# Kernel optimization log

Hardware: AMD Instinct MI355X
Metric: run time of the kernel (lower is better)

## Reference

```python
import jax, jax.numpy as jnp
import numpy as np

B, N, HID = 8, 512, 512
HEADS, HD = 16, 32
FFN, DEMB = 2048, 64
EPS = 1e-5


def layer_norm(x, g, b):
    mu = jnp.mean(x, axis=-1, keepdims=True)
    var = jnp.var(x, axis=-1, keepdims=True)
    return (x - mu) * jax.lax.rsqrt(var + EPS) * g + b


def setup_inputs() -> dict:
    key = jax.random.key(0)
    ks = jax.random.split(key, 16)
    s = lambda fan_in: 1.0 / np.sqrt(fan_in)
    return {
        "x": jax.random.normal(ks[0], (B, N, HID), jnp.float32),
        "distance_features": jax.random.normal(ks[1], (B, N, N, DEMB), jnp.float32),
        "edge_mask": jax.random.randint(ks[2], (B, N, N), 0, 2) > 0,
        "qkv_w": jax.random.uniform(ks[3], (HID, 3 * HID), jnp.float32, -s(HID), s(HID)),
        "qkv_b": jnp.zeros((3 * HID,), jnp.float32),
        "out_w": jax.random.uniform(ks[4], (HID, HID), jnp.float32, -s(HID), s(HID)),
        "out_b": jnp.zeros((HID,), jnp.float32),
        "dist_w": jax.random.uniform(ks[5], (DEMB, HEADS), jnp.float32, -s(DEMB), s(DEMB)),
        "dist_b": jnp.zeros((HEADS,), jnp.float32),
        "ln1_g": jnp.ones((HID,), jnp.float32),
        "ln1_b": jnp.zeros((HID,), jnp.float32),
        "ln2_g": jnp.ones((HID,), jnp.float32),
        "ln2_b": jnp.zeros((HID,), jnp.float32),
        "ff1_w": jax.random.uniform(ks[6], (HID, FFN), jnp.float32, -s(HID), s(HID)),
        "ff1_b": jnp.zeros((FFN,), jnp.float32),
        "ff2_w": jax.random.uniform(ks[7], (FFN, HID), jnp.float32, -s(FFN), s(FFN)),
        "ff2_b": jnp.zeros((HID,), jnp.float32),
    }


def reference(x, distance_features, edge_mask, qkv_w, qkv_b, out_w, out_b,
              dist_w, dist_b, ln1_g, ln1_b, ln2_g, ln2_b,
              ff1_w, ff1_b, ff2_w, ff2_b):
    residual = x
    h = layer_norm(x, ln1_g, ln1_b)
    qkv = h @ qkv_w + qkv_b  # [B,N,3*HID]
    q, k, v = jnp.split(qkv, 3, axis=-1)
    q = q.reshape(B, N, HEADS, HD)
    k = k.reshape(B, N, HEADS, HD)
    v = v.reshape(B, N, HEADS, HD)
    scale = jnp.sqrt(jnp.float32(HD))
    scores = jnp.einsum('bihd,bjhd->bhij', q, k) / scale  # [B,H,N,N]
    bias = distance_features @ dist_w + dist_b  # [B,N,N,H]
    scores = scores + jnp.transpose(bias, (0, 3, 1, 2))
    neg = jnp.finfo(scores.dtype).min
    scores = jnp.where(edge_mask[:, None, :, :], scores, neg)
    attn = jax.nn.softmax(scores, axis=-1)
    ctx = jnp.einsum('bhij,bjhd->bihd', attn, v).reshape(B, N, HID)
    x = residual + ctx @ out_w + out_b
    y = layer_norm(x, ln2_g, ln2_b)
    ff = jax.nn.gelu(y @ ff1_w + ff1_b, approximate=False) @ ff2_w + ff2_b
    return x + ff
```

## Files before the change

kernel.cpp:

```cpp
#include <hip/hip_runtime.h>
#include <cstddef>
#include <cstdint>

#define B_     8
#define N_     512
#define HID_   512
#define HEADS_ 16
#define HD_    32
#define FFN_   2048
#define DEMB_  64
#define ROWS   (B_*N_)

typedef unsigned short u16;
typedef short bf16x8 __attribute__((ext_vector_type(8)));
typedef float f32x4  __attribute__((ext_vector_type(4)));
typedef short short8v __attribute__((ext_vector_type(8)));
typedef short short4v __attribute__((ext_vector_type(4)));

__device__ __forceinline__ u16 f2bf(float f) {
  unsigned u = __float_as_uint(f);
  u += 0x7fffu + ((u >> 16) & 1u);
  return (u16)(u >> 16);
}
__device__ __forceinline__ float bf2f(u16 b) {
  return __uint_as_float(((unsigned)b) << 16);
}

__device__ __forceinline__ void gload16(const void* g, void* l) {
  __builtin_amdgcn_global_load_lds(
      (const __attribute__((address_space(1))) unsigned int*)g,
      (__attribute__((address_space(3))) unsigned int*)l, 16, 0, 0);
}

__device__ __forceinline__ void wt_tile(const float* __restrict__ W,
                                        u16* __restrict__ Wt,
                                        int K, int N, int tt, int tid) {
  __shared__ float tile[32][33];
  const int nt = N / 32;
  const int n0 = (tt % nt) * 32, k0 = (tt / nt) * 32;
  const int tx = tid & 31, ty = tid >> 5;
  #pragma unroll
  for (int i = 0; i < 4; ++i)
    tile[ty + 8 * i][tx] = W[(size_t)(k0 + ty + 8 * i) * N + n0 + tx];
  __syncthreads();
  #pragma unroll
  for (int i = 0; i < 4; ++i) {
    const int n = ty + 8 * i;
    Wt[(size_t)(n0 + n) * K + k0 + tx] = f2bf(tile[tx][n]);
  }
}

__global__ __launch_bounds__(256) void prep_kernel(
    const float* __restrict__ qkv_w, const float* __restrict__ out_w,
    const float* __restrict__ ff1_w, const float* __restrict__ ff2_w,
    u16* __restrict__ qkv_wt, u16* __restrict__ out_wt,
    u16* __restrict__ ff1_wt, u16* __restrict__ ff2_wt,
    const unsigned char* __restrict__ mask, int* __restrict__ flag) {
  const int bid = blockIdx.x, t = threadIdx.x;
  if (bid < 768) {
    wt_tile(qkv_w, qkv_wt, HID_, 3 * HID_, bid, t);
  } else if (bid < 1024) {
    wt_tile(out_w, out_wt, HID_, HID_, bid - 768, t);
  } else if (bid < 2048) {
    wt_tile(ff1_w, ff1_wt, HID_, FFN_, bid - 1024, t);
  } else if (bid < 3072) {
    wt_tile(ff2_w, ff2_wt, FFN_, HID_, bid - 2048, t);
  } else {
    const int idx = (bid - 3072) * 256 + t;
    if ((idx & 3) != 0 && mask[idx] != 0) atomicOr(flag, 1);
  }
}

__global__ __launch_bounds__(256) void ln_kernel(const float* __restrict__ x,
                                                 const float* __restrict__ g,
                                                 const float* __restrict__ bt,
                                                 u16* __restrict__ y) {
  const int lane = threadIdx.x & 63;
  const int row  = blockIdx.x * 4 + (threadIdx.x >> 6);
  const float* xr = x + (size_t)row * HID_;
  float4 v0 = *(const float4*)(xr + lane * 8);
  float4 v1 = *(const float4*)(xr + lane * 8 + 4);
  float s = v0.x + v0.y + v0.z + v0.w + v1.x + v1.y + v1.z + v1.w;
  float q = v0.x*v0.x + v0.y*v0.y + v0.z*v0.z + v0.w*v0.w
          + v1.x*v1.x + v1.y*v1.y + v1.z*v1.z + v1.w*v1.w;
  #pragma unroll
  for (int off = 32; off > 0; off >>= 1) {
    s += __shfl_xor(s, off, 64);
    q += __shfl_xor(q, off, 64);
  }
  const float mean = s * (1.0f / HID_);
  const float var  = q * (1.0f / HID_) - mean * mean;
  const float rs   = rsqrtf(var + 1e-5f);
  const float4 g0 = *(const float4*)(g + lane * 8);
  const float4 g1 = *(const float4*)(g + lane * 8 + 4);
  const float4 b0 = *(const float4*)(bt + lane * 8);
  const float4 b1 = *(const float4*)(bt + lane * 8 + 4);
  short8v o;
  o[0] = (short)f2bf((v0.x - mean) * rs * g0.x + b0.x);
  o[1] = (short)f2bf((v0.y - mean) * rs * g0.y + b0.y);
  o[2] = (short)f2bf((v0.z - mean) * rs * g0.z + b0.z);
  o[3] = (short)f2bf((v0.w - mean) * rs * g0.w + b0.w);
  o[4] = (short)f2bf((v1.x - mean) * rs * g1.x + b1.x);
  o[5] = (short)f2bf((v1.y - mean) * rs * g1.y + b1.y);
  o[6] = (short)f2bf((v1.z - mean) * rs * g1.z + b1.z);
  o[7] = (short)f2bf((v1.w - mean) * rs * g1.w + b1.w);
  *(short8v*)(y + (size_t)row * HID_ + lane * 8) = o;
}

template <int ACT, bool HAS_RES, bool OUT_BF16>
__global__ __launch_bounds__(256) void mfma_gemm(
    const u16* __restrict__ A, const u16* __restrict__ Wt,
    const float* __restrict__ bias, const float* __restrict__ res,
    void* __restrict__ Cout, int N, int K) {
  __shared__ __align__(16) u16 As[128 * 64];
  __shared__ __align__(16) u16 Bs[128 * 64];
  const int t    = threadIdx.x;
  const int wid  = t >> 6, lane = t & 63;
  const int wr   = wid >> 1, wc = wid & 1;
  const int m0   = blockIdx.y * 128, n0 = blockIdx.x * 128;
  const int srow8 = lane >> 3;
  const int sslot = (lane & 7) ^ srow8;

  f32x4 zero = {0.f, 0.f, 0.f, 0.f};
  f32x4 acc[4][4];
  #pragma unroll
  for (int m = 0; m < 4; ++m)
    #pragma unroll
    for (int n = 0; n < 4; ++n) acc[m][n] = zero;

  for (int kt = 0; kt < K; kt += 64) {
    __syncthreads();
    #pragma unroll
    for (int i = 0; i < 4; ++i) {
      const int rbase = wid * 32 + i * 8;
      const int r = rbase + srow8;
      gload16(A  + (size_t)(m0 + r) * K + kt + sslot * 8, &As[rbase * 64]);
      gload16(Wt + (size_t)(n0 + r) * K + kt + sslot * 8, &Bs[rbase * 64]);
    }
    __syncthreads();
    #pragma unroll
    for (int kk = 0; kk < 2; ++kk) {
      bf16x8 a[4], b[4];
      #pragma unroll
      for (int m = 0; m < 4; ++m) {
        const int row = wr * 64 + m * 16 + (lane & 15);
        const int s   = (kk * 4 + (lane >> 4)) ^ (row & 7);
        a[m] = *(const bf16x8*)&As[row * 64 + s * 8];
      }
      #pragma unroll
      for (int n = 0; n < 4; ++n) {
        const int row = wc * 64 + n * 16 + (lane & 15);
        const int s   = (kk * 4 + (lane >> 4)) ^ (row & 7);
        b[n] = *(const bf16x8*)&Bs[row * 64 + s * 8];
      }
      #pragma unroll
      for (int m = 0; m < 4; ++m)
        #pragma unroll
        for (int n = 0; n < 4; ++n)
          acc[m][n] = __builtin_amdgcn_mfma_f32_16x16x32_bf16(
              a[m], b[n], acc[m][n], 0, 0, 0);
    }
  }
  #pragma unroll
  for (int n = 0; n < 4; ++n) {
    const int col = n0 + wc * 64 + n * 16 + (lane & 15);
    const float bb = bias[col];
    #pragma unroll
    for (int m = 0; m < 4; ++m) {
      #pragma unroll
      for (int j = 0; j < 4; ++j) {
        const int row = m0 + wr * 64 + m * 16 + (lane >> 4) * 4 + j;
        float v = acc[m][n][j] + bb;
        if (ACT == 1) v = 0.5f * v * (1.0f + erff(v * 0.70710678118654752f));
        const size_t off = (size_t)row * N + col;
        if (HAS_RES) v += res[off];
        if (OUT_BF16) ((u16*)Cout)[off] = f2bf(v);
        else          ((float*)Cout)[off] = v;
      }
    }
  }
}

__global__ __launch_bounds__(256) void bias_kernel(
    const float* __restrict__ df, const unsigned char* __restrict__ mask8,
    const float* __restrict__ dw, const float* __restrict__ db,
    const int* __restrict__ flag, u16* __restrict__ biasb) {
  __shared__ __align__(16) float dfs[128 * 64];
  __shared__ float wls[64 * 16];
  __shared__ float dbs[16];
  __shared__ unsigned char mbuf[128];
  __shared__ u16 obuf[16][132];

  const int t    = threadIdx.x;
  const int wid  = t >> 6, lane = t & 63;
  const int tile = blockIdx.x & 3;
  const int i    = (blockIdx.x >> 2) & 511;
  const int b    = blockIdx.x >> 11;
  const int j0   = tile * 128;

  const size_t dfbase = (((size_t)b * N_ + i) * N_ + j0) * DEMB_;
  #pragma unroll
  for (int s = 0; s < 8; ++s) {
    const int r0 = wid * 32 + s * 4;
    const int r  = r0 + (lane >> 4);
    const int g  = (lane & 15) ^ (r & 15);
    gload16(df + dfbase + (size_t)r * DEMB_ + g * 4, &dfs[r0 * 64]);
  }
  *(float4*)&wls[t * 4] = ((const float4*)dw)[t];
  if (t < 16) dbs[t] = db[t];
  const int fb = *flag;
  if (t < 128) {
    const size_t midx = ((size_t)b * N_ + i) * N_ + j0 + t;
    mbuf[t] = fb ? (mask8[midx] != 0) : (((const int*)mask8)[midx] != 0);
  }
  __syncthreads();

  bf16x8 bw[2];
  #pragma unroll
  for (int kk = 0; kk < 2; ++kk)
    #pragma unroll
    for (int e = 0; e < 8; ++e) {
      const int k = kk * 32 + (lane >> 4) * 8 + e;
      bw[kk][e] = (short)f2bf(wls[k * 16 + (lane & 15)]);
    }

  f32x4 acc[2] = {{0.f,0.f,0.f,0.f},{0.f,0.f,0.f,0.f}};
  #pragma unroll
  for (int t8 = 0; t8 < 2; ++t8) {
    const int row = wid * 32 + t8 * 16 + (lane & 15);
    #pragma unroll
    for (int kk = 0; kk < 2; ++kk) {
      bf16x8 a;
      #pragma unroll
      for (int gg = 0; gg < 2; ++gg) {
        const int G = kk * 8 + (lane >> 4) * 2 + gg;
        const int p = G ^ (row & 15);
        const float4 v = *(const float4*)&dfs[row * 64 + p * 4];
        a[gg*4+0] = (short)f2bf(v.x); a[gg*4+1] = (short)f2bf(v.y);
        a[gg*4+2] = (short)f2bf(v.z); a[gg*4+3] = (short)f2bf(v.w);
      }
      acc[t8] = __builtin_amdgcn_mfma_f32_16x16x32_bf16(a, bw[kk], acc[t8], 0, 0, 0);
    }
  }

  const int h = lane & 15;
  #pragma unroll
  for (int t8 = 0; t8 < 2; ++t8)
    #pragma unroll
    for (int j = 0; j < 4; ++j) {
      const int jl = wid * 32 + t8 * 16 + (lane >> 4) * 4 + j;
      const float v = acc[t8][j] + dbs[h];
      obuf[h][jl] = f2bf(mbuf[jl] ? v : -1e30f);
    }
  __syncthreads();
  const int h2 = t >> 4, c = t & 15;
  u16* ob = biasb + (((size_t)b * HEADS_ + h2) * N_ + i) * N_ + j0;
  *(short8v*)(ob + c * 8) = *(const short8v*)&obuf[h2][c * 8];
}

__global__ __launch_bounds__(256, 4) void attn_kernel(
    const float* __restrict__ qkv, const u16* __restrict__ biasb,
    u16* __restrict__ ctx) {
  __shared__ union {
    u16 k[N_ * HD_];
    struct {
      float po[3][64][33];
      float pm[3][64];
      float pl[3][64];
    } c;
  } sm;
  const int t    = threadIdx.x;
  const int bx   = blockIdx.x;
  const int b    = bx >> 7;
  const int h    = (bx >> 3) & 15;
  const int iblk = bx & 7;
  const int jq   = t >> 6;
  const int r    = t & 63;
  const int i    = iblk * 64 + r;
  const size_t qbase = (size_t)b * N_ * (3 * HID_);

  for (int idx = t; idx < N_ * 8; idx += 256) {
    const int j = idx >> 3, f = idx & 7;
    const float4 kv = *(const float4*)(qkv + qbase + (size_t)j * (3 * HID_) +
                                       HID_ + h * HD_ + f * 4);
    short4v ks;
    ks[0] = (short)f2bf(kv.x); ks[1] = (short)f2bf(kv.y);
    ks[2] = (short)f2bf(kv.z); ks[3] = (short)f2bf(kv.w);
    *(short4v*)&sm.k[j * HD_ + f * 4] = ks;
  }
  __syncthreads();

  float q[HD_];
  {
    const float* qp = qkv + qbase + (size_t)i * (3 * HID_) + h * HD_;
    #pragma unroll
    for (int f = 0; f < 8; ++f) {
      const float4 v = *(const float4*)(qp + f * 4);
      q[f*4+0] = v.x * 0.17677669529663687f;
      q[f*4+1] = v.y * 0.17677669529663687f;
      q[f*4+2] = v.z * 0.17677669529663687f;
      q[f*4+3] = v.w * 0.17677669529663687f;
    }
  }
  const u16* brow = biasb + (((size_t)b * HEADS_ + h) * N_ + i) * N_ + jq * 128;
  const float* vbase = qkv + qbase + 2 * HID_ + h * HD_;
  float m = -3.0e38f, l = 0.f;
  float o[HD_];
  #pragma unroll
  for (int d = 0; d < HD_; ++d) o[d] = 0.f;

  for (int jc = 0; jc < 128; jc += 8) {
    float s[8];
    const short8v bq = *(const short8v*)(brow + jc);
    #pragma unroll
    for (int e = 0; e < 8; ++e) {
      const int j = jq * 128 + jc + e;
      const u16* kr = &sm.k[j * HD_];
      float s0 = 0.f, s1 = 0.f, s2 = 0.f, s3 = 0.f;
      #pragma unroll
      for (int c = 0; c < 4; ++c) {
        const short8v kk = *(const short8v*)(kr + c * 8);
        s0 += q[c*8+0] * bf2f((u16)kk[0]);
        s1 += q[c*8+1] * bf2f((u16)kk[1]);
        s2 += q[c*8+2] * bf2f((u16)kk[2]);
        s3 += q[c*8+3] * bf2f((u16)kk[3]);
        s0 += q[c*8+4] * bf2f((u16)kk[4]);
        s1 += q[c*8+5] * bf2f((u16)kk[5]);
        s2 += q[c*8+6] * bf2f((u16)kk[6]);
        s3 += q[c*8+7] * bf2f((u16)kk[7]);
      }
      s[e] = (s0 + s1) + (s2 + s3) + bf2f((u16)bq[e]);
    }
    float mc = fmaxf(fmaxf(fmaxf(s[0], s[1]), fmaxf(s[2], s[3])),
                     fmaxf(fmaxf(s[4], s[5]), fmaxf(s[6], s[7])));
    if (mc - m > 8.0f) {
      const float corr = __expf(m - mc);
      l *= corr;
      #pragma unroll
      for (int d = 0; d < HD_; ++d) o[d] *= corr;
      m = mc;
    }
    #pragma unroll
    for (int e = 0; e < 8; ++e) s[e] = __expf(s[e] - m);
    l += ((s[0]+s[1])+(s[2]+s[3])) + ((s[4]+s[5])+(s[6]+s[7]));
    #pragma unroll
    for (int e = 0; e < 8; ++e) {
      const int j = jq * 128 + jc + e;
      const float p = s[e];
      const float4* vr = (const float4*)(vbase + (size_t)j * (3 * HID_));
      #pragma unroll
      for (int c = 0; c < 8; ++c) {
        const float4 vv = vr[c];
        o[c*4+0] += p * vv.x; o[c*4+1] += p * vv.y;
        o[c*4+2] += p * vv.z; o[c*4+3] += p * vv.w;
      }
    }
  }

  __syncthreads();
  if (jq > 0) {
    sm.c.pm[jq-1][r] = m;
    sm.c.pl[jq-1][r] = l;
    #pragma unroll
    for (int d = 0; d < HD_; ++d) sm.c.po[jq-1][r][d] = o[d];
  }
  __syncthreads();
  if (jq == 0) {
    #pragma unroll
    for (int p2 = 0; p2 < 3; ++p2) {
      const float m2 = sm.c.pm[p2][r], l2 = sm.c.pl[p2][r];
      const float mn = fmaxf(m, m2);
      const float c1 = __expf(m - mn), c2 = __expf(m2 - mn);
      l = l * c1 + l2 * c2;
      #pragma unroll
      for (int d = 0; d < HD_; ++d)
        o[d] = o[d] * c1 + sm.c.po[p2][r][d] * c2;
      m = mn;
    }
    const float inv = 1.0f / l;
    u16* cp = ctx + (((size_t)b * N_ + i) * HEADS_ + h) * HD_;
    #pragma unroll
    for (int f = 0; f < 4; ++f) {
      short8v v;
      #pragma unroll
      for (int e = 0; e < 8; ++e) v[e] = (short)f2bf(o[f*8+e] * inv);
      *(short8v*)(cp + f * 8) = v;
    }
  }
}

extern "C" void kernel_launch(void* const* d_in, const int* in_sizes, int n_in,
                              void* d_out, int out_size, void* d_ws, size_t ws_size,
                              hipStream_t stream) {
  const float* x      = (const float*)d_in[0];
  const float* df     = (const float*)d_in[1];
  const unsigned char* mask = (const unsigned char*)d_in[2];
  const float* qkv_w  = (const float*)d_in[3];
  const float* qkv_b  = (const float*)d_in[4];
  const float* out_w  = (const float*)d_in[5];
  const float* out_b  = (const float*)d_in[6];
  const float* dist_w = (const float*)d_in[7];
  const float* dist_b = (const float*)d_in[8];
  const float* ln1_g  = (const float*)d_in[9];
  const float* ln1_b  = (const float*)d_in[10];
  const float* ln2_g  = (const float*)d_in[11];
  const float* ln2_b  = (const float*)d_in[12];
  const float* ff1_w  = (const float*)d_in[13];
  const float* ff1_b  = (const float*)d_in[14];
  const float* ff2_w  = (const float*)d_in[15];
  const float* ff2_b  = (const float*)d_in[16];
  float* out = (float*)d_out;

  char* p = (char*)d_ws;
  auto alloc = [&](size_t bytes) {
    char* r = p;
    p += (bytes + 255) & ~(size_t)255;
    return r;
  };
  float* qkv    = (float*)alloc((size_t)ROWS * 3 * HID_ * 4);
  u16*   biasb  = (u16*)alloc((size_t)B_ * HEADS_ * N_ * N_ * 2);
  float* xa     = (float*)alloc((size_t)ROWS * HID_ * 4);
  u16*   h16    = (u16*)alloc((size_t)ROWS * HID_ * 2);
  u16*   ctx16  = (u16*)alloc((size_t)ROWS * HID_ * 2);
  u16*   y16    = (u16*)alloc((size_t)ROWS * HID_ * 2);
  u16*   ff116  = (u16*)alloc((size_t)ROWS * FFN_ * 2);
  u16*   qkv_wt = (u16*)alloc((size_t)3 * HID_ * HID_ * 2);
  u16*   out_wt = (u16*)alloc((size_t)HID_ * HID_ * 2);
  u16*   ff1_wt = (u16*)alloc((size_t)FFN_ * HID_ * 2);
  u16*   ff2_wt = (u16*)alloc((size_t)HID_ * FFN_ * 2);
  int*   flag   = (int*)alloc(sizeof(int));

  hipMemsetAsync(flag, 0, sizeof(int), stream);
  prep_kernel<<<3328, 256, 0, stream>>>(qkv_w, out_w, ff1_w, ff2_w,
                                        qkv_wt, out_wt, ff1_wt, ff2_wt,
                                        mask, flag);
  ln_kernel<<<ROWS / 4, 256, 0, stream>>>(x, ln1_g, ln1_b, h16);
  mfma_gemm<0, false, false><<<dim3(3 * HID_ / 128, ROWS / 128), 256, 0, stream>>>(
      h16, qkv_wt, qkv_b, nullptr, qkv, 3 * HID_, HID_);
  bias_kernel<<<B_ * N_ * 4, 256, 0, stream>>>(df, mask, dist_w, dist_b, flag, biasb);
  attn_kernel<<<B_ * HEADS_ * 8, 256, 0, stream>>>(qkv, biasb, ctx16);
  mfma_gemm<0, true, false><<<dim3(HID_ / 128, ROWS / 128), 256, 0, stream>>>(
      ctx16, out_wt, out_b, x, xa, HID_, HID_);
  ln_kernel<<<ROWS / 4, 256, 0, stream>>>(xa, ln2_g, ln2_b, y16);
  mfma_gemm<1, false, true><<<dim3(FFN_ / 128, ROWS / 128), 256, 0, stream>>>(
      y16, ff1_wt, ff1_b, nullptr, ff116, FFN_, HID_);
  mfma_gemm<0, true, false><<<dim3(HID_ / 128, ROWS / 128), 256, 0, stream>>>(
      ff116, ff2_wt, ff2_b, xa, out, HID_, FFN_);
}
```

Measured before the change: 431.8 us.

## Stage V and Q in LDS as bf16 and prefetch bias in attention

The attention kernel now converts V to bf16 and stages it in shared memory next to K, so the PV accumulation reads from LDS instead of re-reading fp32 V rows from global memory for every j. Q rows are also loaded cooperatively into shared memory, and the next bias vector is prefetched one iteration ahead. The launch-bounds occupancy hint is dropped because the larger LDS footprint (about 73KB) limits blocks per CU anyway. This adds bf16 rounding of V and lowers occupancy, which could reduce latency hiding.

```diff
diff --git a/kernel.cpp b/kernel.cpp
--- a/kernel.cpp
+++ b/kernel.cpp
@@ -258,11 +258,15 @@
   *(short8v*)(ob + c * 8) = *(const short8v*)&obuf[h2][c * 8];
 }
 
-__global__ __launch_bounds__(256, 4) void attn_kernel(
+__global__ __launch_bounds__(256) void attn_kernel(
     const float* __restrict__ qkv, const u16* __restrict__ biasb,
     u16* __restrict__ ctx) {
-  __shared__ union {
-    u16 k[N_ * HD_];
+  __shared__ __align__(16) union {
+    struct {
+      u16      k[N_ * HD_];
+      unsigned v[N_ * (HD_/2)];
+      float    qs[64][36];
+    } s;
     struct {
       float po[3][64][33];
       float pm[3][64];
@@ -281,41 +285,50 @@
 
   for (int idx = t; idx < N_ * 8; idx += 256) {
     const int j = idx >> 3, f = idx & 7;
-    const float4 kv = *(const float4*)(qkv + qbase + (size_t)j * (3 * HID_) +
-                                       HID_ + h * HD_ + f * 4);
+    const float* base = qkv + qbase + (size_t)j * (3 * HID_) + HID_ + h * HD_ + f * 4;
+    const float4 kv = *(const float4*)base;
+    const float4 vv = *(const float4*)(base + HID_);
     short4v ks;
     ks[0] = (short)f2bf(kv.x); ks[1] = (short)f2bf(kv.y);
     ks[2] = (short)f2bf(kv.z); ks[3] = (short)f2bf(kv.w);
-    *(short4v*)&sm.k[j * HD_ + f * 4] = ks;
+    *(short4v*)&sm.s.k[j * HD_ + f * 4] = ks;
+    uint2 vp;
+    vp.x = (unsigned)f2bf(vv.x) | ((unsigned)f2bf(vv.y) << 16);
+    vp.y = (unsigned)f2bf(vv.z) | ((unsigned)f2bf(vv.w) << 16);
+    *(uint2*)&sm.s.v[j * (HD_/2) + f * 2] = vp;
+  }
+  for (int idx = t; idx < 64 * 8; idx += 256) {
+    const int row = idx >> 3, f = idx & 7;
+    *(float4*)&sm.s.qs[row][f * 4] =
+        *(const float4*)(qkv + qbase + (size_t)(iblk * 64 + row) * (3 * HID_) +
+                         h * HD_ + f * 4);
   }
   __syncthreads();
 
   float q[HD_];
-  {
-    const float* qp = qkv + qbase + (size_t)i * (3 * HID_) + h * HD_;
-    #pragma unroll
-    for (int f = 0; f < 8; ++f) {
-      const float4 v = *(const float4*)(qp + f * 4);
-      q[f*4+0] = v.x * 0.17677669529663687f;
-      q[f*4+1] = v.y * 0.17677669529663687f;
-      q[f*4+2] = v.z * 0.17677669529663687f;
-      q[f*4+3] = v.w * 0.17677669529663687f;
-    }
+  #pragma unroll
+  for (int f = 0; f < 8; ++f) {
+    const float4 v = *(const float4*)&sm.s.qs[r][f * 4];
+    q[f*4+0] = v.x * 0.17677669529663687f;
+    q[f*4+1] = v.y * 0.17677669529663687f;
+    q[f*4+2] = v.z * 0.17677669529663687f;
+    q[f*4+3] = v.w * 0.17677669529663687f;
   }
   const u16* brow = biasb + (((size_t)b * HEADS_ + h) * N_ + i) * N_ + jq * 128;
-  const float* vbase = qkv + qbase + 2 * HID_ + h * HD_;
   float m = -3.0e38f, l = 0.f;
   float o[HD_];
   #pragma unroll
   for (int d = 0; d < HD_; ++d) o[d] = 0.f;
 
+  short8v bq = *(const short8v*)(brow);
   for (int jc = 0; jc < 128; jc += 8) {
+    short8v bqn = bq;
+    if (jc + 8 < 128) bqn = *(const short8v*)(brow + jc + 8);
     float s[8];
-    const short8v bq = *(const short8v*)(brow + jc);
     #pragma unroll
     for (int e = 0; e < 8; ++e) {
       const int j = jq * 128 + jc + e;
-      const u16* kr = &sm.k[j * HD_];
+      const u16* kr = &sm.s.k[j * HD_];
       float s0 = 0.f, s1 = 0.f, s2 = 0.f, s3 = 0.f;
       #pragma unroll
       for (int c = 0; c < 4; ++c) {
@@ -347,14 +360,21 @@
     for (int e = 0; e < 8; ++e) {
       const int j = jq * 128 + jc + e;
       const float p = s[e];
-      const float4* vr = (const float4*)(vbase + (size_t)j * (3 * HID_));
-      #pragma unroll
-      for (int c = 0; c < 8; ++c) {
-        const float4 vv = vr[c];
-        o[c*4+0] += p * vv.x; o[c*4+1] += p * vv.y;
-        o[c*4+2] += p * vv.z; o[c*4+3] += p * vv.w;
-      }
-    }
+      const uint4* vr = (const uint4*)&sm.s.v[j * (HD_/2)];
+      #pragma unroll
+      for (int c4 = 0; c4 < 4; ++c4) {
+        const uint4 pk = vr[c4];
+        o[c4*8+0] += p * __uint_as_float(pk.x << 16);
+        o[c4*8+1] += p * __uint_as_float(pk.x & 0xffff0000u);
+        o[c4*8+2] += p * __uint_as_float(pk.y << 16);
+        o[c4*8+3] += p * __uint_as_float(pk.y & 0xffff0000u);
+        o[c4*8+4] += p * __uint_as_float(pk.z << 16);
+        o[c4*8+5] += p * __uint_as_float(pk.z & 0xffff0000u);
+        o[c4*8+6] += p * __uint_as_float(pk.w << 16);
+        o[c4*8+7] += p * __uint_as_float(pk.w & 0xffff0000u);
+      }
+    }
+    bq = bqn;
   }
 
   __syncthreads();
```

New measurement: 447.8 us. 1.04x slower.
